# Performance work log

Hardware: AMD Instinct MI355X
Metric: run time of the kernel (lower is better)

## Reference

```python
import jax, jax.numpy as jnp
import numpy as np
from jax import lax

B, T, N, D, M, K, H = 16, 96, 256, 128, 1196, 8, 4
HD = D // H  # head dim = 32
TAU_TIME = 2.0


def setup_inputs() -> dict:
    key = jax.random.key(0)
    ks = jax.random.split(key, 12)
    w = lambda k, shp: jax.random.normal(k, shp, jnp.float32) * 0.05
    return {
        "x_scalar": jax.random.normal(ks[0], (B, T, N), jnp.float32),
        "season_q": jax.random.randint(ks[1], (B,), 0, 4),
        "year_q": 2010.0 + 10.0 * jax.random.uniform(ks[2], (B,), jnp.float32),
        "dw_w": w(ks[3], (N, 1, 12)),          # depthwise Conv1d weight (out=N, in/groups=1, k=12)
        "dw_b": jnp.zeros((N,), jnp.float32),
        "pw_w": w(ks[4], (N * D, N)),          # pointwise Conv1d weight (out=N*D, in=N), k=1 squeezed
        "pw_b": jnp.zeros((N * D,), jnp.float32),
        "ln_g": jnp.ones((D,), jnp.float32),
        "ln_b": jnp.zeros((D,), jnp.float32),
        "memory_bank": jax.random.normal(ks[5], (M, N, D), jnp.float32),
        "memory_seasons": jax.random.randint(ks[6], (M,), 0, 4),
        "memory_years": 2010.0 + 10.0 * jax.random.uniform(ks[7], (M,), jnp.float32),
        "in_proj_w": w(ks[8], (3 * D, D)),     # MHA packed q/k/v projection
        "in_proj_b": jnp.zeros((3 * D,), jnp.float32),
        "out_proj_w": w(ks[9], (D, D)),
        "out_proj_b": jnp.zeros((D,), jnp.float32),
        "proj_w": w(ks[10], (D, D)),
        "proj_b": jnp.zeros((D,), jnp.float32),
    }


def _layernorm(x, g, b, eps=1e-5):
    mu = jnp.mean(x, axis=-1, keepdims=True)
    var = jnp.mean((x - mu) ** 2, axis=-1, keepdims=True)
    return (x - mu) * lax.rsqrt(var + eps) * g + b


def _l2norm(x, eps=1e-12):
    n = jnp.sqrt(jnp.sum(x * x, axis=-1, keepdims=True))
    return x / jnp.maximum(n, eps)


def _forward(x_scalar, season_q, year_q, dw_w, dw_b, pw_w, pw_b, ln_g, ln_b,
             memory_bank, memory_seasons, memory_years,
             in_proj_w, in_proj_b, out_proj_w, out_proj_b, proj_w, proj_b):
    b, t, n = x_scalar.shape
    d = ln_g.shape[0]
    m = memory_bank.shape[0]

    # --- TemporalEncoder ---
    x = jnp.transpose(x_scalar, (0, 2, 1))  # (b, n, t): permute(0,2,3,1).reshape with d_input=1
    x = lax.conv_general_dilated(
        x, dw_w, window_strides=(1,), padding=[(6, 6)],
        dimension_numbers=("NCH", "OIH", "NCH"), feature_group_count=n)
    x = jax.nn.gelu(x + dw_b[:, None], approximate=False)      # (b, n, t+1)
    x = jnp.einsum("bct,oc->bot", x, pw_w) + pw_b[:, None]     # pointwise 1x1 conv -> (b, n*d, t+1)
    x = jax.nn.gelu(x, approximate=False)
    x = jnp.mean(x, axis=-1).reshape(b, n, d)                  # adaptive avg pool to 1
    q = _layernorm(x, ln_g, ln_b)                              # (b, n, d)

    # --- retrieve ---
    qf = _l2norm(q.reshape(b, n * d))
    memf = _l2norm(memory_bank.reshape(m, n * d))
    sim = qf @ memf.T                                          # (b, m)
    smask = (season_q[:, None] == memory_seasons[None, :]).astype(sim.dtype)
    sim = sim * smask + (1.0 - smask) * (-10000.0)
    dy = jnp.abs(year_q[:, None] - memory_years[None, :])
    diversity = 1.0 - jnp.exp(-dy / max(TAU_TIME, 1e-4))
    sim = sim * (0.5 + 0.5 * diversity)
    _, idx = lax.top_k(sim, K)                                 # (b, K)
    retrieved = memory_bank[idx]                               # (b, K, n, d)

    # --- cross attention: query (b*n, 1, d) vs kv (b*n, K, d) ---
    Wq, Wk, Wv = in_proj_w[:d], in_proj_w[d:2 * d], in_proj_w[2 * d:]
    bq, bk, bv = in_proj_b[:d], in_proj_b[d:2 * d], in_proj_b[2 * d:]
    kv = jnp.transpose(retrieved, (0, 2, 1, 3))                # (b, n, K, d)
    qp = (jnp.einsum("bnd,ed->bne", q, Wq) + bq).reshape(b, n, H, HD)
    kp = (jnp.einsum("bnkd,ed->bnke", kv, Wk) + bk).reshape(b, n, K, H, HD)
    vp = (jnp.einsum("bnkd,ed->bnke", kv, Wv) + bv).reshape(b, n, K, H, HD)
    scores = jnp.einsum("bnhe,bnkhe->bnhk", qp, kp) / np.sqrt(HD)
    attn = jax.nn.softmax(scores, axis=-1)
    ctx = jnp.einsum("bnhk,bnkhe->bnhe", attn, vp).reshape(b, n, d)
    out = jnp.einsum("bnd,ed->bne", ctx, out_proj_w) + out_proj_b
    out = jnp.einsum("bnd,ed->bne", out, proj_w) + proj_b
    return out, q


def reference(x_scalar, season_q, year_q, dw_w, dw_b, pw_w, pw_b, ln_g, ln_b,
              memory_bank, memory_seasons, memory_years,
              in_proj_w, in_proj_b, out_proj_w, out_proj_b, proj_w, proj_b):
    return _forward(x_scalar, season_q, year_q, dw_w, dw_b, pw_w, pw_b, ln_g, ln_b,
                    memory_bank, memory_seasons, memory_years,
                    in_proj_w, in_proj_b, out_proj_w, out_proj_b, proj_w, proj_b)
```

## Files before the change

### kernel.cpp

```cpp
#include <hip/hip_runtime.h>

typedef _Float16 f16x8 __attribute__((ext_vector_type(8)));
typedef _Float16 f16x4 __attribute__((ext_vector_type(4)));
typedef float    f32x4 __attribute__((ext_vector_type(4)));

__device__ __forceinline__ float gelu_f(float x) {
    float z  = 0.70710678118654752440f * x;
    float az = fabsf(z);
    float t  = 1.0f / fmaf(0.3275911f, az, 1.0f);
    float e  = __expf(-az * az);
    float p  = t * fmaf(t, fmaf(t, fmaf(t, fmaf(t, 1.061405429f, -1.453152027f),
                                        1.421413741f), -0.284496736f), 0.254829592f);
    float er = fmaf(-p, e, 1.0f);
    float s  = (z < 0.0f) ? -er : er;
    return 0.5f * x * (1.0f + s);
}

__device__ __forceinline__ void gload16(const void* g, void* l) {
    __builtin_amdgcn_global_load_lds(
        (const __attribute__((address_space(1))) unsigned int*)g,
        (__attribute__((address_space(3))) unsigned int*)l, 16, 0, 0);
}

__global__ void conv_kernel(const float* __restrict__ xs, const float* __restrict__ dww,
                            const float* __restrict__ dwb, _Float16* __restrict__ Gt)
{
    int b = blockIdx.x, t = blockIdx.y, n = threadIdx.x;
    float g = 0.f;
    if (t < 97) {
        float y = 0.f;
        #pragma unroll
        for (int j = 0; j < 12; ++j) {
            int tt = t + j - 6;
            if (tt >= 0 && tt < 96)
                y += dww[n*12 + j] * xs[((size_t)b*96 + tt)*256 + n];
        }
        g = gelu_f(y + dwb[n]);
    }
    Gt[((size_t)b*128 + t)*256 + n] = (_Float16)g;
}

__global__ void cvt_pw_kernel(const float* __restrict__ src, _Float16* __restrict__ dst,
                              const float* __restrict__ ipw, const float* __restrict__ opw,
                              const float* __restrict__ pjw, const float* __restrict__ opb,
                              const float* __restrict__ pjb, _Float16* __restrict__ wAll,
                              float* __restrict__ zp, _Float16* __restrict__ Wcf,
                              float* __restrict__ bc)
{
    int bid = blockIdx.x, tid = threadIdx.x;
    if (bid < 8192) {
        size_t i = ((size_t)bid*256 + tid) * 4;
        float4 v = *(const float4*)&src[i];
        f16x4 o; o[0] = (_Float16)v.x; o[1] = (_Float16)v.y; o[2] = (_Float16)v.z; o[3] = (_Float16)v.w;
        *(f16x4*)&dst[i] = o;
    } else if (bid < 8512) {
        int i = (bid - 8192)*256 + tid;
        float v = (i < 49152) ? ipw[i] : (i < 65536 ? opw[i - 49152] : pjw[i - 65536]);
        wAll[i] = (_Float16)v;
    } else if (bid < 8532) {
        int i = (bid - 8512)*256 + tid;
        if (i < 5087) {
            float4 z = {0.f, 0.f, 0.f, 0.f};
            *(float4*)&zp[i*4] = z;
        }
    } else {
        int e = (bid - 8532)*2 + (tid >> 7);
        int c = tid & 127;
        float acc = 0.f;
        for (int d = 0; d < 128; ++d)
            acc = fmaf(pjw[e*128 + d], opw[d*128 + c], acc);
        Wcf[e*128 + c] = (_Float16)acc;
        if (c == 0) {
            float s = pjb[e];
            for (int d = 0; d < 128; ++d)
                s = fmaf(pjw[e*128 + d], opb[d], s);
            bc[e] = s;
        }
    }
}

__global__ __launch_bounds__(256) void pw_kernel(const _Float16* __restrict__ W,
                                                 const _Float16* __restrict__ Gt,
                                                 const float* __restrict__ pwb,
                                                 const float* __restrict__ lng,
                                                 const float* __restrict__ lnb,
                                                 float* __restrict__ qout,
                                                 _Float16* __restrict__ qh,
                                                 _Float16* __restrict__ qhT,
                                                 _Float16* __restrict__ qloT,
                                                 float* __restrict__ qss)
{
    __shared__ __align__(16) _Float16 As[2][128][32];
    __shared__ __align__(16) _Float16 Bs[2][128][32];

    int x = blockIdx.x;
    int xcd = x & 7, ii = x >> 3;
    int ob = xcd * 32 + (ii >> 4);
    int b  = ii & 15;
    const _Float16* Arow = W  + (size_t)ob * 128 * 256;
    const _Float16* Brow = Gt + (size_t)b  * 128 * 256;

    int tid = threadIdx.x, w = tid >> 6, l = tid & 63, lr = l & 15, lk = l >> 4;
    int wr = w >> 1, wc = w & 1;
    int rsw = (lr >> 1) & 3;

    f32x4 acc[4][4];
    #pragma unroll
    for (int i = 0; i < 4; ++i)
        #pragma unroll
        for (int j = 0; j < 4; ++j)
            acc[i][j] = f32x4{0.f, 0.f, 0.f, 0.f};

    auto stage = [&](int buf, int k0) {
        #pragma unroll
        for (int j = 0; j < 2; ++j) {
            int chunk = tid + j*256;
            int row = chunk >> 2;
            int co  = (chunk & 3) * 8;
            int cos = ((chunk & 3) ^ ((chunk >> 3) & 3)) * 8;
            gload16(&Arow[row*256 + k0 + cos], &As[buf][row][co]);
            gload16(&Brow[row*256 + k0 + cos], &Bs[buf][row][co]);
        }
    };

    stage(0, 0);
    __syncthreads();
    for (int ks = 0; ks < 8; ++ks) {
        int cur = ks & 1;
        if (ks < 7) stage(cur ^ 1, (ks + 1) * 32);
        f16x8 a[4], bb[4];
        #pragma unroll
        for (int i = 0; i < 4; ++i)
            a[i]  = *(const f16x8*)&As[cur][wr*64 + i*16 + lr][(lk ^ rsw)*8];
        #pragma unroll
        for (int j = 0; j < 4; ++j)
            if (wc == 0 || j < 3)
                bb[j] = *(const f16x8*)&Bs[cur][wc*64 + j*16 + lr][(lk ^ rsw)*8];
        #pragma unroll
        for (int i = 0; i < 4; ++i)
            #pragma unroll
            for (int j = 0; j < 4; ++j)
                if (wc == 0 || j < 3)
                    acc[i][j] = __builtin_amdgcn_mfma_f32_16x16x32_f16(bb[j], a[i], acc[i][j], 0, 0, 0);
        __syncthreads();
    }

    float (*red)[2] = reinterpret_cast<float(*)[2]>(&As[0][0][0]);
    #pragma unroll
    for (int i = 0; i < 4; ++i) {
        int og = ob*128 + wr*64 + i*16 + lr;
        float pbv = pwb[og];
        float s = 0.f;
        if (wc == 0) {
            #pragma unroll
            for (int j = 0; j < 4; ++j)
                #pragma unroll
                for (int r = 0; r < 4; ++r)
                    s += gelu_f(acc[i][j][r] + pbv);
        } else {
            #pragma unroll
            for (int j = 0; j < 2; ++j)
                #pragma unroll
                for (int r = 0; r < 4; ++r)
                    s += gelu_f(acc[i][j][r] + pbv);
            if (lk == 0) s += gelu_f(acc[i][2][0] + pbv);
        }
        s += __shfl_xor(s, 16, 64);
        s += __shfl_xor(s, 32, 64);
        if (lk == 0) red[wr*64 + i*16 + lr][wc] = s;
    }
    __syncthreads();

    if (w == 0) {
        float x0 = (red[l][0]      + red[l][1])      * (1.f/97.f);
        float x1 = (red[64 + l][0] + red[64 + l][1]) * (1.f/97.f);
        float sm = x0 + x1;
        #pragma unroll
        for (int m = 1; m < 64; m <<= 1) sm += __shfl_xor(sm, m, 64);
        float mu = sm * (1.f/128.f);
        float d0 = x0 - mu, d1 = x1 - mu;
        float vv = d0*d0 + d1*d1;
        #pragma unroll
        for (int m = 1; m < 64; m <<= 1) vv += __shfl_xor(vv, m, 64);
        float rs = 1.0f / sqrtf(vv * (1.f/128.f) + 1e-5f);
        float q0 = d0*rs*lng[l]      + lnb[l];
        float q1 = d1*rs*lng[64 + l] + lnb[64 + l];
        size_t bn = (size_t)b*256 + ob;
        qout[bn*128 + l]      = q0;
        qout[bn*128 + 64 + l] = q1;
        _Float16 h0 = (_Float16)q0, h1 = (_Float16)q1;
        qh[bn*128 + l]       = h0;
        qh[bn*128 + 64 + l]  = h1;
        int ch0 = ob*4 + (l >> 5);
        int sub = b*32 + ((l >> 3) & 3)*8 + (l & 7);
        qhT [ch0*512 + sub]       = h0;
        qhT [(ch0 + 2)*512 + sub] = h1;
        qloT[ch0*512 + sub]       = (_Float16)(q0 - (float)h0);
        qloT[(ch0 + 2)*512 + sub] = (_Float16)(q1 - (float)h1);
        float ss = q0*q0 + q1*q1;
        #pragma unroll
        for (int m = 1; m < 64; m <<= 1) ss += __shfl_xor(ss, m, 64);
        if (l == 0) atomicAdd(&qss[b], ss);
    }
}

__global__ __launch_bounds__(256) void simgemm_kernel(const _Float16* __restrict__ qhT,
                                                      const _Float16* __restrict__ qloT,
                                                      const float* __restrict__ mem,
                                                      float* __restrict__ dotp,
                                                      float* __restrict__ mn2)
{
    __shared__ __align__(16) float Ms[2][16][256];
    __shared__ f32x4 redls[4][64];
    __shared__ float redn[4][16];

    int tid = threadIdx.x, w = tid >> 6, l = tid & 63, lr = l & 15, lk = l >> 4;
    int m0 = blockIdx.y * 16;
    int kwin = blockIdx.x * 1024;
    int rowm = m0 + lr;

    auto stage = [&](int buf, int sw) {
        #pragma unroll
        for (int j = 0; j < 4; ++j) {
            int r = w*4 + j;
            int rowg = m0 + r; if (rowg > 1195) rowg = 1195;
            const float* src = mem + (size_t)rowg*32768 + kwin + sw*256 + (l ^ (r & 7))*4;
            gload16(src, &Ms[buf][r][0]);
        }
    };

    f32x4 acc_a = {0.f,0.f,0.f,0.f}, acc_b = {0.f,0.f,0.f,0.f};
    float nacc = 0.f;

    stage(0, 0);
    __syncthreads();
    for (int sw = 0; sw < 4; ++sw) {
        int cur = sw & 1;
        if (sw < 3) stage(cur ^ 1, sw + 1);
        #pragma unroll
        for (int cc = 0; cc < 2; ++cc) {
            int kl = w*64 + cc*32;
            int s0 = (kl + lk*8) >> 2;
            float4 v0 = *(const float4*)&Ms[cur][lr][(s0       ^ (lr & 7))*4];
            float4 v1 = *(const float4*)&Ms[cur][lr][((s0 + 1) ^ (lr & 7))*4];
            int chunk = (kwin + sw*256 + kl) >> 5;
            int fo = lr*4 + lk;
            f16x8 ah = ((const f16x8*)(qhT  + (size_t)chunk*512))[fo];
            f16x8 al = ((const f16x8*)(qloT + (size_t)chunk*512))[fo];
            float e0 = v0.x, e1 = v0.y, e2 = v0.z, e3 = v0.w;
            float e4 = v1.x, e5 = v1.y, e6 = v1.z, e7 = v1.w;
            f16x8 bh;
            bh[0]=(_Float16)e0; bh[1]=(_Float16)e1; bh[2]=(_Float16)e2; bh[3]=(_Float16)e3;
            bh[4]=(_Float16)e4; bh[5]=(_Float16)e5; bh[6]=(_Float16)e6; bh[7]=(_Float16)e7;
            nacc = fmaf(e0,e0, fmaf(e1,e1, fmaf(e2,e2, fmaf(e3,e3, nacc))));
            nacc = fmaf(e4,e4, fmaf(e5,e5, fmaf(e6,e6, fmaf(e7,e7, nacc))));
            acc_a = __builtin_amdgcn_mfma_f32_16x16x32_f16(ah, bh, acc_a, 0, 0, 0);
            acc_b = __builtin_amdgcn_mfma_f32_16x16x32_f16(al, bh, acc_b, 0, 0, 0);
        }
        __syncthreads();
    }

    nacc += __shfl_xor(nacc, 16, 64);
    nacc += __shfl_xor(nacc, 32, 64);

    f32x4 tot = acc_a + acc_b;
    redls[w][l] = tot;
    if (lk == 0) redn[w][lr] = nacc;
    __syncthreads();
    if (w == 0) {
        tot = redls[0][l];
        tot += redls[1][l]; tot += redls[2][l]; tot += redls[3][l];
        if (rowm < 1196) {
            #pragma unroll
            for (int r = 0; r < 4; ++r)
                atomicAdd(&dotp[(lk*4 + r)*1196 + rowm], tot[r]);
            if (lk == 0)
                atomicAdd(&mn2[rowm], redn[0][lr] + redn[1][lr] + redn[2][lr] + redn[3][lr]);
        }
    }
}

__global__ void topk_kernel(const float* __restrict__ dotp, const float* __restrict__ mn2,
                            const float* __restrict__ qss, const int* __restrict__ seaq,
                            const float* __restrict__ yq, const int* __restrict__ seam,
                            const float* __restrict__ ym, int* __restrict__ idx)
{
    __shared__ float sc[1216];
    int b = blockIdx.x, lane = threadIdx.x;
    float qn = fmaxf(sqrtf(qss[b]), 1e-12f);
    int sq = seaq[b];
    float yqv = yq[b];
    for (int m = lane; m < 1216; m += 64) {
        float v = -3e38f;
        if (m < 1196) {
            float s = dotp[b*1196 + m] / (qn * fmaxf(sqrtf(mn2[m]), 1e-12f));
            if (seam[m] != sq) s = -10000.0f;
            float dy = fabsf(yqv - ym[m]);
            v = s * (1.0f - 0.5f * expf(-0.5f * dy));
        }
        sc[m] = v;
    }
    __syncthreads();
    for (int kk = 0; kk < 8; ++kk) {
        float bv = -3e38f; int bi = 0x7fffffff;
        for (int m = lane; m < 1216; m += 64) {
            float v = sc[m];
            if (v > bv) { bv = v; bi = m; }
        }
        #pragma unroll
        for (int mk = 1; mk < 64; mk <<= 1) {
            float ov = __shfl_xor(bv, mk, 64);
            int   oi = __shfl_xor(bi, mk, 64);
            if (ov > bv || (ov == bv && oi < bi)) { bv = ov; bi = oi; }
        }
        if (lane == 0) { idx[b*8 + kk] = bi; sc[bi] = -3e38f; }
        __syncthreads();
    }
}

__global__ __launch_bounds__(256) void qkv_kernel(const _Float16* __restrict__ qh,
                                                  const float* __restrict__ memb,
                                                  const int* __restrict__ idx,
                                                  const _Float16* __restrict__ wAll,
                                                  const float* __restrict__ ipb,
                                                  _Float16* __restrict__ qp,
                                                  _Float16* __restrict__ kp,
                                                  _Float16* __restrict__ vp)
{
    int bid = blockIdx.x;
    int tid = threadIdx.x, w = tid >> 6, l = tid & 63, lr = l & 15, lk = l >> 4;

    if (bid < 64) {
        int r0 = bid * 64 + w * 16;
        const _Float16* Ah = qh + (size_t)(r0 + lr)*128 + lk*8;
        f32x4 acc[8];
        #pragma unroll
        for (int j = 0; j < 8; ++j) acc[j] = f32x4{0.f, 0.f, 0.f, 0.f};
        #pragma unroll
        for (int k0 = 0; k0 < 128; k0 += 32) {
            f16x8 a = *(const f16x8*)&Ah[k0];
            #pragma unroll
            for (int j = 0; j < 8; ++j) {
                f16x8 bb = *(const f16x8*)&wAll[(j*16 + lr)*128 + k0 + lk*8];
                acc[j] = __builtin_amdgcn_mfma_f32_16x16x32_f16(a, bb, acc[j], 0, 0, 0);
            }
        }
        #pragma unroll
        for (int j = 0; j < 8; ++j) {
            #pragma unroll
            for (int r = 0; r < 4; ++r) {
                int row = r0 + lk*4 + r, col = j*16 + lr;
                qp[(size_t)row*128 + col] = (_Float16)(acc[j][r] + ipb[col]);
            }
        }
    } else {
        int blk = bid - 64;
        int r0 = blk * 64 + w * 16;
        int bk = (blk * 64) >> 8;
        int row = idx[bk];
        const float* Af = memb + (size_t)row*32768 + ((r0 & 255) + lr)*128 + lk*8;
        const _Float16* Wk = wAll + 16384;
        const _Float16* Wv = wAll + 32768;

        f32x4 acck[8], accv[8];
        #pragma unroll
        for (int j = 0; j < 8; ++j) { acck[j] = f32x4{0.f,0.f,0.f,0.f}; accv[j] = f32x4{0.f,0.f,0.f,0.f}; }
        #pragma unroll
        for (int k0 = 0; k0 < 128; k0 += 32) {
            float4 v0 = *(const float4*)&Af[k0];
            float4 v1 = *(const float4*)&Af[k0 + 4];
            f16x8 a;
            a[0]=(_Float16)v0.x; a[1]=(_Float16)v0.y; a[2]=(_Float16)v0.z; a[3]=(_Float16)v0.w;
            a[4]=(_Float16)v1.x; a[5]=(_Float16)v1.y; a[6]=(_Float16)v1.z; a[7]=(_Float16)v1.w;
            #pragma unroll
            for (int j = 0; j < 8; ++j) {
                f16x8 bk_ = *(const f16x8*)&Wk[(j*16 + lr)*128 + k0 + lk*8];
                acck[j] = __builtin_amdgcn_mfma_f32_16x16x32_f16(a, bk_, acck[j], 0, 0, 0);
                f16x8 bv_ = *(const f16x8*)&Wv[(j*16 + lr)*128 + k0 + lk*8];
                accv[j] = __builtin_amdgcn_mfma_f32_16x16x32_f16(a, bv_, accv[j], 0, 0, 0);
            }
        }
        #pragma unroll
        for (int j = 0; j < 8; ++j) {
            #pragma unroll
            for (int r = 0; r < 4; ++r) {
                int row2 = r0 + lk*4 + r, col = j*16 + lr;
                kp[(size_t)row2*128 + col] = (_Float16)(acck[j][r] + ipb[128 + col]);
                vp[(size_t)row2*128 + col] = (_Float16)(accv[j][r] + ipb[256 + col]);
            }
        }
    }
}

__global__ void attn_kernel(const _Float16* __restrict__ qp, const _Float16* __restrict__ kp,
                            const _Float16* __restrict__ vp, const _Float16* __restrict__ Wc,
                            const float* __restrict__ bc, float* __restrict__ outp)
{
    __shared__ float ctxs[128];
    int bn = blockIdx.x;
    int b = bn >> 8, n = bn & 255;
    int tid = threadIdx.x;
    float qv = (float)qp[(size_t)bn*128 + tid];
    float sc[8];
    #pragma unroll
    for (int k = 0; k < 8; ++k) {
        float p = qv * (float)kp[(((size_t)(b*8 + k)*256 + n)*128) + tid];
        #pragma unroll
        for (int m = 1; m < 32; m <<= 1) p += __shfl_xor(p, m, 64);
        sc[k] = p * 0.17677669529663687f;
    }
    float mx = sc[0];
    #pragma unroll
    for (int k = 1; k < 8; ++k) mx = fmaxf(mx, sc[k]);
    float den = 0.f;
    #pragma unroll
    for (int k = 0; k < 8; ++k) { sc[k] = expf(sc[k] - mx); den += sc[k]; }
    float inv = 1.f / den;
    float c = 0.f;
    #pragma unroll
    for (int k = 0; k < 8; ++k)
        c += sc[k] * (float)vp[(((size_t)(b*8 + k)*256 + n)*128) + tid];
    ctxs[tid] = c * inv;
    __syncthreads();

    float s = bc[tid];
    const f16x8* wrow = (const f16x8*)&Wc[(size_t)tid*128];
    #pragma unroll
    for (int c0 = 0; c0 < 16; ++c0) {
        f16x8 wv = wrow[c0];
        #pragma unroll
        for (int u = 0; u < 8; ++u)
            s = fmaf(ctxs[c0*8 + u], (float)wv[u], s);
    }
    outp[(size_t)bn*128 + tid] = s;
}

extern "C" void kernel_launch(void* const* d_in, const int* in_sizes, int n_in,
                              void* d_out, int out_size, void* d_ws, size_t ws_size,
                              hipStream_t stream)
{
    const float* x_scalar = (const float*)d_in[0];
    const int*   season_q = (const int*)d_in[1];
    const float* year_q   = (const float*)d_in[2];
    const float* dw_w     = (const float*)d_in[3];
    const float* dw_b     = (const float*)d_in[4];
    const float* pw_w     = (const float*)d_in[5];
    const float* pw_b     = (const float*)d_in[6];
    const float* ln_g     = (const float*)d_in[7];
    const float* ln_b     = (const float*)d_in[8];
    const float* memb     = (const float*)d_in[9];
    const int*   mseas    = (const int*)d_in[10];
    const float* myear    = (const float*)d_in[11];
    const float* ipw      = (const float*)d_in[12];
    const float* ipb      = (const float*)d_in[13];
    const float* opw      = (const float*)d_in[14];
    const float* opb      = (const float*)d_in[15];
    const float* pjw      = (const float*)d_in[16];
    const float* pjb      = (const float*)d_in[17];

    char* wsb = (char*)d_ws;
    _Float16* Wf   = (_Float16*)(wsb + 0);
    _Float16* Gt   = (_Float16*)(wsb + 16777216);
    _Float16* qloT = (_Float16*)(wsb + 17825792);
    _Float16* qh   = (_Float16*)(wsb + 19922944);
    float*    qss  = (float*)   (wsb + 20971520);
    float*    dotp = (float*)   (wsb + 20971584);
    float*    mn2  = (float*)   (wsb + 21048128);
    int*      idxb = (int*)     (wsb + 21052928);
    _Float16* qp   = (_Float16*)(wsb + 29442048);
    _Float16* kp   = (_Float16*)(wsb + 30490624);
    _Float16* vp   = (_Float16*)(wsb + 38879232);
    _Float16* Wcf  = (_Float16*)(wsb + 48316416);
    float*    bc   = (float*)   (wsb + 48349184);
    _Float16* wAll = (_Float16*)(wsb + 49364992);
    _Float16* qhT  = (_Float16*)(wsb + 49528832);

    float* outp = (float*)d_out;
    float* qout = (float*)d_out + 524288;

    cvt_pw_kernel<<<8596, 256, 0, stream>>>(pw_w, Wf, ipw, opw, pjw, opb, pjb, wAll,
                                            (float*)(wsb + 20971520), Wcf, bc);
    conv_kernel<<<dim3(16, 128), 256, 0, stream>>>(x_scalar, dw_w, dw_b, Gt);

    pw_kernel<<<4096, 256, 0, stream>>>(Wf, Gt, pw_b, ln_g, ln_b, qout, qh, qhT, qloT, qss);

    simgemm_kernel<<<dim3(32, 75), 256, 0, stream>>>(qhT, qloT, memb, dotp, mn2);
    topk_kernel<<<16, 64, 0, stream>>>(dotp, mn2, qss, season_q, year_q, mseas, myear, idxb);

    qkv_kernel<<<576, 256, 0, stream>>>(qh, memb, idxb, wAll, ipb, qp, kp, vp);

    attn_kernel<<<4096, 128, 0, stream>>>(qp, kp, vp, Wcf, bc, outp);
}
```

Before: 198.9 us.

## Pre-swizzle pointwise GEMM operands into MFMA fragment order and drop LDS staging

The pointwise weight conversion and the depthwise conv output now write fp16 data directly in per-lane MFMA fragment order. This lets pw_kernel load each operand fragment with one coalesced 16-byte global load and skip the LDS double buffer and its per-step barriers. The cost is that every wave reads operands straight from global memory or L2 with no shared-memory reuse across the waves of a block, so latency is hidden only by the 2x loop unroll and by occupancy. The layout-scattering writes in the conv and conversion kernels are also less contiguous than before.

```diff
diff --git a/kernel.cpp b/kernel.cpp
--- a/kernel.cpp
+++ b/kernel.cpp
@@ -23,7 +23,7 @@
 }
 
 __global__ void conv_kernel(const float* __restrict__ xs, const float* __restrict__ dww,
-                            const float* __restrict__ dwb, _Float16* __restrict__ Gt)
+                            const float* __restrict__ dwb, _Float16* __restrict__ Bf)
 {
     int b = blockIdx.x, t = blockIdx.y, n = threadIdx.x;
     float g = 0.f;
@@ -37,7 +37,9 @@
         }
         g = gelu_f(y + dwb[n]);
     }
-    Gt[((size_t)b*128 + t)*256 + n] = (_Float16)g;
+    int ks = n >> 5, lk = (n >> 3) & 3, e = n & 7;
+    int jj = t >> 4, lr = t & 15;
+    Bf[(((size_t)b*8 + ks)*8 + jj)*512 + (lk*16 + lr)*8 + e] = (_Float16)g;
 }
 
 __global__ void cvt_pw_kernel(const float* __restrict__ src, _Float16* __restrict__ dst,
@@ -48,23 +50,32 @@
                               float* __restrict__ bc)
 {
     int bid = blockIdx.x, tid = threadIdx.x;
-    if (bid < 8192) {
-        size_t i = ((size_t)bid*256 + tid) * 4;
-        float4 v = *(const float4*)&src[i];
-        f16x4 o; o[0] = (_Float16)v.x; o[1] = (_Float16)v.y; o[2] = (_Float16)v.z; o[3] = (_Float16)v.w;
-        *(f16x4*)&dst[i] = o;
-    } else if (bid < 8512) {
-        int i = (bid - 8192)*256 + tid;
+    if (bid < 2048) {
+        int ob = bid >> 3, ks = bid & 7;
+        #pragma unroll
+        for (int s = 0; s < 2; ++s) {
+            int slot = tid + s*256;
+            int ii = slot >> 6, l2 = slot & 63, lr = l2 & 15, lk = l2 >> 4;
+            const float* sp = src + (size_t)(ob*128 + ii*16 + lr)*256 + ks*32 + lk*8;
+            float4 v0 = *(const float4*)sp;
+            float4 v1 = *(const float4*)(sp + 4);
+            f16x8 o;
+            o[0]=(_Float16)v0.x; o[1]=(_Float16)v0.y; o[2]=(_Float16)v0.z; o[3]=(_Float16)v0.w;
+            o[4]=(_Float16)v1.x; o[5]=(_Float16)v1.y; o[6]=(_Float16)v1.z; o[7]=(_Float16)v1.w;
+            *(f16x8*)&dst[(((size_t)ob*8 + ks)*8 + ii)*512 + (size_t)l2*8] = o;
+        }
+    } else if (bid < 2368) {
+        int i = (bid - 2048)*256 + tid;
         float v = (i < 49152) ? ipw[i] : (i < 65536 ? opw[i - 49152] : pjw[i - 65536]);
         wAll[i] = (_Float16)v;
-    } else if (bid < 8532) {
-        int i = (bid - 8512)*256 + tid;
+    } else if (bid < 2388) {
+        int i = (bid - 2368)*256 + tid;
         if (i < 5087) {
             float4 z = {0.f, 0.f, 0.f, 0.f};
             *(float4*)&zp[i*4] = z;
         }
     } else {
-        int e = (bid - 8532)*2 + (tid >> 7);
+        int e = (bid - 2388)*2 + (tid >> 7);
         int c = tid & 127;
         float acc = 0.f;
         for (int d = 0; d < 128; ++d)
@@ -79,8 +90,8 @@
     }
 }
 
-__global__ __launch_bounds__(256) void pw_kernel(const _Float16* __restrict__ W,
-                                                 const _Float16* __restrict__ Gt,
+__global__ __launch_bounds__(256) void pw_kernel(const _Float16* __restrict__ Af,
+                                                 const _Float16* __restrict__ Bf,
                                                  const float* __restrict__ pwb,
                                                  const float* __restrict__ lng,
                                                  const float* __restrict__ lnb,
@@ -90,19 +101,17 @@
                                                  _Float16* __restrict__ qloT,
                                                  float* __restrict__ qss)
 {
-    __shared__ __align__(16) _Float16 As[2][128][32];
-    __shared__ __align__(16) _Float16 Bs[2][128][32];
+    __shared__ float red[128][2];
 
     int x = blockIdx.x;
     int xcd = x & 7, ii = x >> 3;
     int ob = xcd * 32 + (ii >> 4);
     int b  = ii & 15;
-    const _Float16* Arow = W  + (size_t)ob * 128 * 256;
-    const _Float16* Brow = Gt + (size_t)b  * 128 * 256;
-
     int tid = threadIdx.x, w = tid >> 6, l = tid & 63, lr = l & 15, lk = l >> 4;
     int wr = w >> 1, wc = w & 1;
-    int rsw = (lr >> 1) & 3;
+
+    const f16x8* Ap = (const f16x8*)(Af + (size_t)ob*8*8*512) + l;
+    const f16x8* Bp = (const f16x8*)(Bf + (size_t)b *8*8*512) + l;
 
     f32x4 acc[4][4];
     #pragma unroll
@@ -111,41 +120,24 @@
         for (int j = 0; j < 4; ++j)
             acc[i][j] = f32x4{0.f, 0.f, 0.f, 0.f};
 
-    auto stage = [&](int buf, int k0) {
-        #pragma unroll
-        for (int j = 0; j < 2; ++j) {
-            int chunk = tid + j*256;
-            int row = chunk >> 2;
-            int co  = (chunk & 3) * 8;
-            int cos = ((chunk & 3) ^ ((chunk >> 3) & 3)) * 8;
-            gload16(&Arow[row*256 + k0 + cos], &As[buf][row][co]);
-            gload16(&Brow[row*256 + k0 + cos], &Bs[buf][row][co]);
-        }
-    };
-
-    stage(0, 0);
-    __syncthreads();
+    #pragma unroll 2
     for (int ks = 0; ks < 8; ++ks) {
-        int cur = ks & 1;
-        if (ks < 7) stage(cur ^ 1, (ks + 1) * 32);
         f16x8 a[4], bb[4];
         #pragma unroll
         for (int i = 0; i < 4; ++i)
-            a[i]  = *(const f16x8*)&As[cur][wr*64 + i*16 + lr][(lk ^ rsw)*8];
+            a[i] = Ap[(ks*8 + wr*4 + i)*64];
         #pragma unroll
         for (int j = 0; j < 4; ++j)
             if (wc == 0 || j < 3)
-                bb[j] = *(const f16x8*)&Bs[cur][wc*64 + j*16 + lr][(lk ^ rsw)*8];
+                bb[j] = Bp[(ks*8 + wc*4 + j)*64];
         #pragma unroll
         for (int i = 0; i < 4; ++i)
             #pragma unroll
             for (int j = 0; j < 4; ++j)
                 if (wc == 0 || j < 3)
                     acc[i][j] = __builtin_amdgcn_mfma_f32_16x16x32_f16(bb[j], a[i], acc[i][j], 0, 0, 0);
-        __syncthreads();
-    }
-
-    float (*red)[2] = reinterpret_cast<float(*)[2]>(&As[0][0][0]);
+    }
+
     #pragma unroll
     for (int i = 0; i < 4; ++i) {
         int og = ob*128 + wr*64 + i*16 + lr;
@@ -459,8 +451,8 @@
     const float* pjb      = (const float*)d_in[17];
 
     char* wsb = (char*)d_ws;
-    _Float16* Wf   = (_Float16*)(wsb + 0);
-    _Float16* Gt   = (_Float16*)(wsb + 16777216);
+    _Float16* Afrag= (_Float16*)(wsb + 0);
+    _Float16* Bfrag= (_Float16*)(wsb + 16777216);
     _Float16* qloT = (_Float16*)(wsb + 17825792);
     _Float16* qh   = (_Float16*)(wsb + 19922944);
     float*    qss  = (float*)   (wsb + 20971520);
@@ -478,11 +470,11 @@
     float* outp = (float*)d_out;
     float* qout = (float*)d_out + 524288;
 
-    cvt_pw_kernel<<<8596, 256, 0, stream>>>(pw_w, Wf, ipw, opw, pjw, opb, pjb, wAll,
+    cvt_pw_kernel<<<2452, 256, 0, stream>>>(pw_w, Afrag, ipw, opw, pjw, opb, pjb, wAll,
                                             (float*)(wsb + 20971520), Wcf, bc);
-    conv_kernel<<<dim3(16, 128), 256, 0, stream>>>(x_scalar, dw_w, dw_b, Gt);
-
-    pw_kernel<<<4096, 256, 0, stream>>>(Wf, Gt, pw_b, ln_g, ln_b, qout, qh, qhT, qloT, qss);
+    conv_kernel<<<dim3(16, 128), 256, 0, stream>>>(x_scalar, dw_w, dw_b, Bfrag);
+
+    pw_kernel<<<4096, 256, 0, stream>>>(Afrag, Bfrag, pw_b, ln_g, ln_b, qout, qh, qhT, qloT, qss);
 
     simgemm_kernel<<<dim3(32, 75), 256, 0, stream>>>(qhT, qloT, memb, dotp, mn2);
     topk_kernel<<<16, 64, 0, stream>>>(dotp, mn2, qss, season_q, year_q, mseas, myear, idxb);
```

After: 208.0 us. 4.6% more time.
